# Performance work log

Measured on AMD Instinct MI355X. Metric: run time of the kernel, lower is better.

## Reference

```python
import jax, jax.numpy as jnp
import numpy as np

D_MODEL = 1024
N_HEAD = 16
B, C, S = 4, 4, 1024


def setup_inputs() -> dict:
    key = jax.random.key(0)
    ks = jax.random.split(key, 5)
    d = D_MODEL
    x = jax.random.normal(ks[0], (B, C, S, d), dtype=jnp.float32)
    scale = 1.0 / np.sqrt(d).astype(np.float32)

    def lin(k):
        return jax.random.normal(k, (d, d), dtype=jnp.float32) * scale

    return {
        "x": x,
        "wq": lin(ks[1]), "bq": jnp.zeros((d,), jnp.float32),
        "wk": lin(ks[2]), "bk": jnp.zeros((d,), jnp.float32),
        "wv": lin(ks[3]), "bv": jnp.zeros((d,), jnp.float32),
        "wo": lin(ks[4]), "bo": jnp.zeros((d,), jnp.float32),
    }


def reference(x, wq, bq, wk, bk, wv, bv, wo, bo):
    b, c, s, d = x.shape
    dh = d // N_HEAD
    nh = N_HEAD * c  # channels folded into heads, as in torch .view

    def proj(w, bias):
        # nn.Linear: y = x @ w.T + b  (w stored as [out, in])
        y = jnp.einsum('bcsd,ed->bcse', x, w) + bias
        # view(B, -1, n_head*C, d_head).transpose(1, 2) -> (B, nh, S, dh)
        return jnp.swapaxes(y.reshape(b, -1, nh, dh), 1, 2)

    # NOTE: original multiplies query by sqrt(d_head) (kept faithfully)
    q = proj(wq, bq) * jnp.sqrt(jnp.asarray(dh, x.dtype))
    k = proj(wk, bk)
    v = proj(wv, bv)

    attn = jax.nn.softmax(jnp.einsum('bhqd,bhkd->bhqk', q, k), axis=-1)
    o = jnp.einsum('bhqk,bhkd->bhqd', attn, v)          # (B, nh, S, dh)
    o = jnp.swapaxes(o, 1, 2).reshape(b, -1, N_HEAD * dh)  # (B, S*C, d)
    o = jnp.einsum('bnd,ed->bne', o, wo) + bo
    return o.reshape(b, c, -1, d)  # (B, C, S, d)
```

## Files before the change

### kernel.cpp

```cpp
#include <hip/hip_runtime.h>
#include <stdint.h>

typedef unsigned short u16;
typedef _Float16 f16;
typedef __attribute__((ext_vector_type(8))) _Float16 f16x8;
typedef __attribute__((ext_vector_type(4))) float f32x4;

__device__ __forceinline__ float exp2fast(float x) {
  return __builtin_amdgcn_exp2f(x);
}

__device__ __forceinline__ f32x4 mfma16(f16x8 a, f16x8 b, f32x4 c) {
  return __builtin_amdgcn_mfma_f32_16x16x32_f16(a, b, c, 0, 0, 0);
}

__device__ __forceinline__ u16 f2h(float f) {
  return __builtin_bit_cast(u16, (f16)f);
}

__device__ __forceinline__ void gld16(const void* g, void* l) {
  __builtin_amdgcn_global_load_lds(
      (const __attribute__((address_space(1))) unsigned int*)g,
      (__attribute__((address_space(3))) unsigned int*)l,
      16, 0, 0);
}

__global__ __launch_bounds__(256) void cvt_f32_f16(const float* __restrict__ in,
                                                   u16* __restrict__ out, int n4) {
  int stride = gridDim.x * blockDim.x;
  for (int i = blockIdx.x * blockDim.x + threadIdx.x; i < n4; i += stride) {
    float4 v = reinterpret_cast<const float4*>(in)[i];
    ushort4 o;
    o.x = f2h(v.x); o.y = f2h(v.y); o.z = f2h(v.z); o.w = f2h(v.w);
    reinterpret_cast<ushort4*>(out)[i] = o;
  }
}

struct GemmCore {
  u16* As;
  u16* Bs;
  const u16 *aS0, *aS1, *bS0, *bS1;
  u16 *aD0, *aD1, *bD0, *bD1;
  int aoff[4], boff[4];
};

__device__ __forceinline__ void core_init(GemmCore& c, u16* AsBase, u16* BsBase,
                                          const u16* A, const u16* B,
                                          int m0, int n0, int tid) {
  const int lane = tid & 63;
  const int wid = tid >> 6;
  const int wr = wid >> 1, wc = wid & 1;
  const int qd = lane >> 4, lm = lane & 15;

  c.As = AsBase; c.Bs = BsBase;
  const int srow = wid * 32 + (lane >> 2);
  const int sgran = (lane & 3) ^ ((lane >> 3) & 3);
  c.aS0 = A + (size_t)(m0 + srow) * 1024 + sgran * 8;
  c.aS1 = c.aS0 + (size_t)16 * 1024;
  c.bS0 = B + (size_t)(n0 + srow) * 1024 + sgran * 8;
  c.bS1 = c.bS0 + (size_t)16 * 1024;
  c.aD0 = AsBase + wid * 1024;       c.aD1 = c.aD0 + 512;
  c.bD0 = BsBase + wid * 1024;       c.bD1 = c.bD0 + 512;

  const int rg = (qd ^ ((lm >> 1) & 3)) * 8;
#pragma unroll
  for (int i = 0; i < 4; ++i) c.aoff[i] = (wr * 64 + i * 16 + lm) * 32 + rg;
#pragma unroll
  for (int j = 0; j < 4; ++j) c.boff[j] = (wc * 64 + j * 16 + lm) * 32 + rg;
}

__device__ __forceinline__ void core_stage(GemmCore& c, int buf) {
  const int d = buf * 4096;
  gld16(c.aS0, c.aD0 + d);
  gld16(c.aS1, c.aD1 + d);
  gld16(c.bS0, c.bD0 + d);
  gld16(c.bS1, c.bD1 + d);
}

__device__ __forceinline__ void core_advance(GemmCore& c) {
  c.aS0 += 32; c.aS1 += 32; c.bS0 += 32; c.bS1 += 32;
}

__device__ __forceinline__ void core_mfma(GemmCore& c, int buf, f32x4 (&acc)[4][4]) {
  const u16* aB = c.As + buf * 4096;
  const u16* bB = c.Bs + buf * 4096;
  f16x8 af[4], bf[4];
#pragma unroll
  for (int i = 0; i < 4; ++i)
    af[i] = *reinterpret_cast<const f16x8*>(aB + c.aoff[i]);
#pragma unroll
  for (int j = 0; j < 4; ++j)
    bf[j] = *reinterpret_cast<const f16x8*>(bB + c.boff[j]);
#pragma unroll
  for (int i = 0; i < 4; ++i)
#pragma unroll
    for (int j = 0; j < 4; ++j)
      acc[i][j] = mfma16(af[i], bf[j], acc[i][j]);
}

__global__ __launch_bounds__(256) void proj_qkv(
    const u16* __restrict__ xb,
    const u16* __restrict__ wqh, const u16* __restrict__ wkh, const u16* __restrict__ wvh,
    const float* __restrict__ bq, const float* __restrict__ bk, const float* __restrict__ bv,
    u16* __restrict__ Qf, u16* __restrict__ Kf, u16* __restrict__ Vt) {
  const int mat = blockIdx.z;
  const u16* __restrict__ w = (mat == 0) ? wqh : (mat == 1) ? wkh : wvh;
  const float* __restrict__ bias = (mat == 0) ? bq : (mat == 1) ? bk : bv;
  const int m0 = blockIdx.x * 128;
  const int n0 = blockIdx.y * 128;

  __shared__ __align__(16) u16 As[2][128 * 32];
  __shared__ __align__(16) u16 Bs[2][128 * 32];

  const int tid = threadIdx.x;
  const int lane = tid & 63;
  const int wid = tid >> 6;
  const int wr = wid >> 1, wc = wid & 1;
  const int qd = lane >> 4, lm = lane & 15;

  GemmCore c;
  core_init(c, &As[0][0], &Bs[0][0], xb, w, m0, n0, tid);

  f32x4 acc[4][4];
#pragma unroll
  for (int i = 0; i < 4; ++i)
#pragma unroll
    for (int j = 0; j < 4; ++j) acc[i][j] = (f32x4){0.f, 0.f, 0.f, 0.f};

  core_stage(c, 0);
  __syncthreads();

  int buf = 0;
  for (int kt = 0; kt < 31; ++kt) {
    core_advance(c);
    core_stage(c, buf ^ 1);
    core_mfma(c, buf, acc);
    __syncthreads();
    buf ^= 1;
  }
  core_mfma(c, buf, acc);

  const float scale = (mat == 0) ? 11.5415603f : 1.0f;
#pragma unroll
  for (int i = 0; i < 4; ++i) {
#pragma unroll
    for (int r = 0; r < 4; ++r) {
      int R = m0 + wr * 64 + i * 16 + qd * 4 + r;
      int bb = R >> 12, n = R & 4095;
      int cc = n >> 10, s = n & 1023;
      int rb = s & 3, t = s >> 2;
      int m = cc * 256 + t;
#pragma unroll
      for (int j = 0; j < 4; ++j) {
        int e = n0 + wc * 64 + j * 16 + lm;
        int head = e >> 6, jj = e & 63;
        int h = rb * 16 + head;
        float val = (acc[i][j][r] + bias[e]) * scale;
        u16 hv = f2h(val);
        if (mat == 2) {
          Vt[(((size_t)bb * 64 + h) * 64 + jj) * 1024 + m] = hv;
        } else {
          size_t idx = (((size_t)bb * 64 + h) * 1024 + m) * 64 + jj;
          if (mat == 0) Qf[idx] = hv;
          else          Kf[idx] = hv;
        }
      }
    }
  }
}

__device__ __forceinline__ f16x8 lds_frag(const u16* base, int row, int blk) {
  return *reinterpret_cast<const f16x8*>(base + row * 64 + ((blk ^ (row & 7)) << 3));
}

__device__ __forceinline__ void stage_kv(const u16* __restrict__ Kh,
                                         const u16* __restrict__ Vh, int kc,
                                         u16* KsB, u16* VsB, int wv, int lane) {
  const int l8 = lane >> 3, sl = lane & 7;
  const int rb = wv * 16;
#pragma unroll
  for (int it = 0; it < 2; ++it) {
    int row = rb + it * 8 + l8;
    int gsl = sl ^ l8;
    gld16(Kh + (size_t)(kc * 64 + row) * 64 + gsl * 8, KsB + (rb + it * 8) * 64);
    gld16(Vh + (size_t)row * 1024 + kc * 64 + gsl * 8, VsB + (rb + it * 8) * 64);
  }
}

__global__ __launch_bounds__(256) void attn_kernel(
    const u16* __restrict__ Qf, const u16* __restrict__ Kf,
    const u16* __restrict__ Vt, u16* __restrict__ Of) {
  const int wgid = (blockIdx.x & 7) * 256 + (blockIdx.x >> 3);
  const int bh = wgid >> 3;
  const int m0 = (wgid & 7) * 128;
  const int b = bh >> 6, h = bh & 63;
  const int tid = threadIdx.x, lane = tid & 63, wv = tid >> 6;
  const int qd = lane >> 4, lm = lane & 15;

  __shared__ __align__(16) u16 Ks[2][64 * 64];
  __shared__ __align__(16) u16 Vs[2][64 * 64];

  const size_t hb = (size_t)(b * 64 + h);
  const u16* __restrict__ Qh = Qf + hb * 65536;
  const u16* __restrict__ Kh = Kf + hb * 65536;
  const u16* __restrict__ Vh = Vt + hb * 65536;

  f16x8 qf[2][2];
#pragma unroll
  for (int im = 0; im < 2; ++im)
#pragma unroll
    for (int ks = 0; ks < 2; ++ks)
      qf[im][ks] = *reinterpret_cast<const f16x8*>(
          Qh + (size_t)(m0 + wv * 32 + im * 16 + lm) * 64 + ks * 32 + qd * 8);

  f32x4 oa[2][4];
  float mrow[2] = {-1e30f, -1e30f};
  float lrow[2] = {0.f, 0.f};
#pragma unroll
  for (int im = 0; im < 2; ++im)
#pragma unroll
    for (int jf = 0; jf < 4; ++jf) oa[im][jf] = (f32x4){0.f, 0.f, 0.f, 0.f};

  stage_kv(Kh, Vh, 0, &Ks[0][0], &Vs[0][0], wv, lane);

  for (int kc = 0; kc < 16; ++kc) {
    const int buf = kc & 1;
    __syncthreads();
    if (kc + 1 < 16) stage_kv(Kh, Vh, kc + 1, &Ks[buf ^ 1][0], &Vs[buf ^ 1][0], wv, lane);

    f32x4 sc[2][4];
#pragma unroll
    for (int im = 0; im < 2; ++im)
#pragma unroll
      for (int nf = 0; nf < 4; ++nf) sc[im][nf] = (f32x4){0.f, 0.f, 0.f, 0.f};
#pragma unroll
    for (int ks = 0; ks < 2; ++ks) {
      f16x8 kfr[4];
#pragma unroll
      for (int nf = 0; nf < 4; ++nf)
        kfr[nf] = lds_frag(&Ks[buf][0], nf * 16 + lm, ks * 4 + qd);
#pragma unroll
      for (int im = 0; im < 2; ++im)
#pragma unroll
        for (int nf = 0; nf < 4; ++nf)
          sc[im][nf] = mfma16(kfr[nf], qf[im][ks], sc[im][nf]);
    }

    unsigned int pk[2][8];
#pragma unroll
    for (int im = 0; im < 2; ++im) {
      float pm = sc[im][0][0];
#pragma unroll
      for (int nf = 0; nf < 4; ++nf)
#pragma unroll
        for (int r = 0; r < 4; ++r) pm = fmaxf(pm, sc[im][nf][r]);
      pm = fmaxf(pm, __shfl_xor(pm, 16));
      pm = fmaxf(pm, __shfl_xor(pm, 32));
      if (__all(pm <= mrow[im] + 8.0f)) {
        float mn = mrow[im];
        float s = 0.f;
#pragma unroll
        for (int nf = 0; nf < 4; ++nf) {
          float p0 = exp2fast(sc[im][nf][0] - mn);
          float p1 = exp2fast(sc[im][nf][1] - mn);
          float p2 = exp2fast(sc[im][nf][2] - mn);
          float p3 = exp2fast(sc[im][nf][3] - mn);
          s += (p0 + p1) + (p2 + p3);
          pk[im][2 * nf + 0] = __builtin_bit_cast(unsigned int, __builtin_amdgcn_cvt_pkrtz(p0, p1));
          pk[im][2 * nf + 1] = __builtin_bit_cast(unsigned int, __builtin_amdgcn_cvt_pkrtz(p2, p3));
        }
        s += __shfl_xor(s, 16);
        s += __shfl_xor(s, 32);
        lrow[im] += s;
      } else {
        float mn = fmaxf(mrow[im], pm);
        float corr = exp2fast(mrow[im] - mn);
        mrow[im] = mn;
        float s = 0.f;
#pragma unroll
        for (int nf = 0; nf < 4; ++nf) {
          float p0 = exp2fast(sc[im][nf][0] - mn);
          float p1 = exp2fast(sc[im][nf][1] - mn);
          float p2 = exp2fast(sc[im][nf][2] - mn);
          float p3 = exp2fast(sc[im][nf][3] - mn);
          s += (p0 + p1) + (p2 + p3);
          pk[im][2 * nf + 0] = __builtin_bit_cast(unsigned int, __builtin_amdgcn_cvt_pkrtz(p0, p1));
          pk[im][2 * nf + 1] = __builtin_bit_cast(unsigned int, __builtin_amdgcn_cvt_pkrtz(p2, p3));
        }
        s += __shfl_xor(s, 16);
        s += __shfl_xor(s, 32);
        lrow[im] = lrow[im] * corr + s;
#pragma unroll
        for (int r = 0; r < 4; ++r) {
          float cb = __shfl(corr, qd * 4 + r);
#pragma unroll
          for (int jf = 0; jf < 4; ++jf) oa[im][jf][r] *= cb;
        }
      }
    }

#pragma unroll
    for (int ks = 0; ks < 2; ++ks) {
      f16x8 vfr[4];
#pragma unroll
      for (int jf = 0; jf < 4; ++jf)
        vfr[jf] = lds_frag(&Vs[buf][0], jf * 16 + lm, ks * 4 + qd);
#pragma unroll
      for (int im = 0; im < 2; ++im) {
        union { unsigned int w[4]; f16x8 hv; } pa;
#pragma unroll
        for (int w = 0; w < 4; ++w) {
          int srcl = (((2 * qd + (w >> 1)) & 3) << 4) + lm;
          unsigned int a0 = __shfl(pk[im][2 * (2 * ks + 0) + (w & 1)], srcl);
          unsigned int a1 = __shfl(pk[im][2 * (2 * ks + 1) + (w & 1)], srcl);
          pa.w[w] = (qd & 2) ? a1 : a0;
        }
#pragma unroll
        for (int jf = 0; jf < 4; ++jf)
          oa[im][jf] = mfma16(pa.hv, vfr[jf], oa[im][jf]);
      }
    }
  }

  const int rb = h >> 4, head = h & 15;
#pragma unroll
  for (int im = 0; im < 2; ++im) {
#pragma unroll
    for (int r = 0; r < 4; ++r) {
      float lb = __shfl(lrow[im], qd * 4 + r);
      float inv = 1.0f / lb;
      int mq = m0 + wv * 32 + im * 16 + qd * 4 + r;
      int c = mq >> 8, t = mq & 255;
      int s = t * 4 + rb;
      int n = c * 1024 + s;
#pragma unroll
      for (int jf = 0; jf < 4; ++jf) {
        int j = jf * 16 + lm;
        int f = head * 64 + j;
        Of[((size_t)b * 4096 + n) * 1024 + f] = f2h(oa[im][jf][r] * inv);
      }
    }
  }
}

__global__ __launch_bounds__(256) void out_gemm(
    const u16* __restrict__ Of, const u16* __restrict__ woh,
    const float* __restrict__ bo, float* __restrict__ out) {
  const int m0 = blockIdx.x * 128;
  const int n0 = blockIdx.y * 128;

  __shared__ __align__(16) u16 As[2][128 * 32];
  __shared__ __align__(16) u16 Bs[2][128 * 32];

  const int tid = threadIdx.x;
  const int lane = tid & 63;
  const int wid = tid >> 6;
  const int wr = wid >> 1, wc = wid & 1;
  const int qd = lane >> 4, lm = lane & 15;

  GemmCore c;
  core_init(c, &As[0][0], &Bs[0][0], Of, woh, m0, n0, tid);

  f32x4 acc[4][4];
#pragma unroll
  for (int i = 0; i < 4; ++i)
#pragma unroll
    for (int j = 0; j < 4; ++j) acc[i][j] = (f32x4){0.f, 0.f, 0.f, 0.f};

  core_stage(c, 0);
  __syncthreads();

  int buf = 0;
  for (int kt = 0; kt < 31; ++kt) {
    core_advance(c);
    core_stage(c, buf ^ 1);
    core_mfma(c, buf, acc);
    __syncthreads();
    buf ^= 1;
  }
  core_mfma(c, buf, acc);

#pragma unroll
  for (int i = 0; i < 4; ++i) {
#pragma unroll
    for (int r = 0; r < 4; ++r) {
      int R = m0 + wr * 64 + i * 16 + qd * 4 + r;
#pragma unroll
      for (int j = 0; j < 4; ++j) {
        int e = n0 + wc * 64 + j * 16 + lm;
        out[(size_t)R * 1024 + e] = acc[i][j][r] + bo[e];
      }
    }
  }
}

extern "C" void kernel_launch(void* const* d_in, const int* in_sizes, int n_in,
                              void* d_out, int out_size, void* d_ws, size_t ws_size,
                              hipStream_t stream) {
  const float* x  = (const float*)d_in[0];
  const float* wq = (const float*)d_in[1];
  const float* bq = (const float*)d_in[2];
  const float* wk = (const float*)d_in[3];
  const float* bk = (const float*)d_in[4];
  const float* wv = (const float*)d_in[5];
  const float* bv = (const float*)d_in[6];
  const float* wo = (const float*)d_in[7];
  const float* bo = (const float*)d_in[8];
  float* out = (float*)d_out;

  char* ws = (char*)d_ws;
  u16* xb  = (u16*)(ws + 0);
  u16* wqh = (u16*)(ws + 33554432);
  u16* wkh = (u16*)(ws + 35651584);
  u16* wvh = (u16*)(ws + 37748736);
  u16* woh = (u16*)(ws + 39845888);
  u16* Qfb = (u16*)(ws + 41943040);
  u16* Kfb = (u16*)(ws + 75497472);
  u16* Vtb = (u16*)(ws + 109051904);
  u16* Ofb = (u16*)(ws + 142606336);

  cvt_f32_f16<<<4096, 256, 0, stream>>>(x,  xb,  16777216 / 4);
  cvt_f32_f16<<<1024, 256, 0, stream>>>(wq, wqh, 1048576 / 4);
  cvt_f32_f16<<<1024, 256, 0, stream>>>(wk, wkh, 1048576 / 4);
  cvt_f32_f16<<<1024, 256, 0, stream>>>(wv, wvh, 1048576 / 4);
  cvt_f32_f16<<<1024, 256, 0, stream>>>(wo, woh, 1048576 / 4);

  proj_qkv<<<dim3(128, 8, 3), 256, 0, stream>>>(xb, wqh, wkh, wvh, bq, bk, bv,
                                                Qfb, Kfb, Vtb);
  attn_kernel<<<2048, 256, 0, stream>>>(Qfb, Kfb, Vtb, Ofb);
  out_gemm<<<dim3(128, 8), 256, 0, stream>>>(Ofb, woh, bo, out);
}
```

Baseline: 433.7 us.

## Single-buffer GEMM LDS, merge weight conversions, add MFMA priority hints

Both GEMM kernels drop LDS double buffering for a single buffer with two barriers per k-step, halving shared memory so more blocks can be resident per CU, at the cost of no longer overlapping loads with MFMA inside a block. The four weight conversion launches become one launch that picks its matrix from blockIdx.y, cutting launch overhead. The attention kernel wraps its MFMA sections in s_setprio hints so waves issuing matrix work get scheduling priority over waves doing softmax.

```diff
diff --git a/kernel.cpp b/kernel.cpp
--- a/kernel.cpp
+++ b/kernel.cpp
@@ -36,9 +36,25 @@
   }
 }
 
+struct Ptr8 {
+  const float *s0, *s1, *s2, *s3;
+  u16 *d0, *d1, *d2, *d3;
+};
+__global__ __launch_bounds__(256) void cvt4_f32_f16(Ptr8 p, int n4) {
+  const float* in = (blockIdx.y == 0) ? p.s0 : (blockIdx.y == 1) ? p.s1
+                    : (blockIdx.y == 2) ? p.s2 : p.s3;
+  u16* out = (blockIdx.y == 0) ? p.d0 : (blockIdx.y == 1) ? p.d1
+             : (blockIdx.y == 2) ? p.d2 : p.d3;
+  int stride = gridDim.x * blockDim.x;
+  for (int i = blockIdx.x * blockDim.x + threadIdx.x; i < n4; i += stride) {
+    float4 v = reinterpret_cast<const float4*>(in)[i];
+    ushort4 o;
+    o.x = f2h(v.x); o.y = f2h(v.y); o.z = f2h(v.z); o.w = f2h(v.w);
+    reinterpret_cast<ushort4*>(out)[i] = o;
+  }
+}
+
 struct GemmCore {
-  u16* As;
-  u16* Bs;
   const u16 *aS0, *aS1, *bS0, *bS1;
   u16 *aD0, *aD1, *bD0, *bD1;
   int aoff[4], boff[4];
@@ -52,7 +68,6 @@
   const int wr = wid >> 1, wc = wid & 1;
   const int qd = lane >> 4, lm = lane & 15;
 
-  c.As = AsBase; c.Bs = BsBase;
   const int srow = wid * 32 + (lane >> 2);
   const int sgran = (lane & 3) ^ ((lane >> 3) & 3);
   c.aS0 = A + (size_t)(m0 + srow) * 1024 + sgran * 8;
@@ -69,28 +84,26 @@
   for (int j = 0; j < 4; ++j) c.boff[j] = (wc * 64 + j * 16 + lm) * 32 + rg;
 }
 
-__device__ __forceinline__ void core_stage(GemmCore& c, int buf) {
-  const int d = buf * 4096;
-  gld16(c.aS0, c.aD0 + d);
-  gld16(c.aS1, c.aD1 + d);
-  gld16(c.bS0, c.bD0 + d);
-  gld16(c.bS1, c.bD1 + d);
+__device__ __forceinline__ void core_stage(GemmCore& c) {
+  gld16(c.aS0, c.aD0);
+  gld16(c.aS1, c.aD1);
+  gld16(c.bS0, c.bD0);
+  gld16(c.bS1, c.bD1);
 }
 
 __device__ __forceinline__ void core_advance(GemmCore& c) {
   c.aS0 += 32; c.aS1 += 32; c.bS0 += 32; c.bS1 += 32;
 }
 
-__device__ __forceinline__ void core_mfma(GemmCore& c, int buf, f32x4 (&acc)[4][4]) {
-  const u16* aB = c.As + buf * 4096;
-  const u16* bB = c.Bs + buf * 4096;
+__device__ __forceinline__ void core_mfma(GemmCore& c, const u16* AsBase, const u16* BsBase,
+                                          f32x4 (&acc)[4][4]) {
   f16x8 af[4], bf[4];
 #pragma unroll
   for (int i = 0; i < 4; ++i)
-    af[i] = *reinterpret_cast<const f16x8*>(aB + c.aoff[i]);
+    af[i] = *reinterpret_cast<const f16x8*>(AsBase + c.aoff[i]);
 #pragma unroll
   for (int j = 0; j < 4; ++j)
-    bf[j] = *reinterpret_cast<const f16x8*>(bB + c.boff[j]);
+    bf[j] = *reinterpret_cast<const f16x8*>(BsBase + c.boff[j]);
 #pragma unroll
   for (int i = 0; i < 4; ++i)
 #pragma unroll
@@ -109,8 +122,8 @@
   const int m0 = blockIdx.x * 128;
   const int n0 = blockIdx.y * 128;
 
-  __shared__ __align__(16) u16 As[2][128 * 32];
-  __shared__ __align__(16) u16 Bs[2][128 * 32];
+  __shared__ __align__(16) u16 As[128 * 32];
+  __shared__ __align__(16) u16 Bs[128 * 32];
 
   const int tid = threadIdx.x;
   const int lane = tid & 63;
@@ -119,7 +132,7 @@
   const int qd = lane >> 4, lm = lane & 15;
 
   GemmCore c;
-  core_init(c, &As[0][0], &Bs[0][0], xb, w, m0, n0, tid);
+  core_init(c, As, Bs, xb, w, m0, n0, tid);
 
   f32x4 acc[4][4];
 #pragma unroll
@@ -127,18 +140,14 @@
 #pragma unroll
     for (int j = 0; j < 4; ++j) acc[i][j] = (f32x4){0.f, 0.f, 0.f, 0.f};
 
-  core_stage(c, 0);
-  __syncthreads();
-
-  int buf = 0;
-  for (int kt = 0; kt < 31; ++kt) {
-    core_advance(c);
-    core_stage(c, buf ^ 1);
-    core_mfma(c, buf, acc);
+  core_stage(c);
+
+  for (int kt = 0; kt < 32; ++kt) {
     __syncthreads();
-    buf ^= 1;
-  }
-  core_mfma(c, buf, acc);
+    core_mfma(c, As, Bs, acc);
+    __syncthreads();
+    if (kt + 1 < 32) { core_advance(c); core_stage(c); }
+  }
 
   const float scale = (mat == 0) ? 11.5415603f : 1.0f;
 #pragma unroll
@@ -233,6 +242,7 @@
     for (int im = 0; im < 2; ++im)
 #pragma unroll
       for (int nf = 0; nf < 4; ++nf) sc[im][nf] = (f32x4){0.f, 0.f, 0.f, 0.f};
+    __builtin_amdgcn_s_setprio(1);
 #pragma unroll
     for (int ks = 0; ks < 2; ++ks) {
       f16x8 kfr[4];
@@ -245,6 +255,7 @@
         for (int nf = 0; nf < 4; ++nf)
           sc[im][nf] = mfma16(kfr[nf], qf[im][ks], sc[im][nf]);
     }
+    __builtin_amdgcn_s_setprio(0);
 
     unsigned int pk[2][8];
 #pragma unroll
@@ -315,9 +326,11 @@
           unsigned int a1 = __shfl(pk[im][2 * (2 * ks + 1) + (w & 1)], srcl);
           pa.w[w] = (qd & 2) ? a1 : a0;
         }
+        __builtin_amdgcn_s_setprio(1);
 #pragma unroll
         for (int jf = 0; jf < 4; ++jf)
           oa[im][jf] = mfma16(pa.hv, vfr[jf], oa[im][jf]);
+        __builtin_amdgcn_s_setprio(0);
       }
     }
   }
@@ -349,8 +362,8 @@
   const int m0 = blockIdx.x * 128;
   const int n0 = blockIdx.y * 128;
 
-  __shared__ __align__(16) u16 As[2][128 * 32];
-  __shared__ __align__(16) u16 Bs[2][128 * 32];
+  __shared__ __align__(16) u16 As[128 * 32];
+  __shared__ __align__(16) u16 Bs[128 * 32];
 
   const int tid = threadIdx.x;
   const int lane = tid & 63;
@@ -359,7 +372,7 @@
   const int qd = lane >> 4, lm = lane & 15;
 
   GemmCore c;
-  core_init(c, &As[0][0], &Bs[0][0], Of, woh, m0, n0, tid);
+  core_init(c, As, Bs, Of, woh, m0, n0, tid);
 
   f32x4 acc[4][4];
 #pragma unroll
@@ -367,18 +380,14 @@
 #pragma unroll
     for (int j = 0; j < 4; ++j) acc[i][j] = (f32x4){0.f, 0.f, 0.f, 0.f};
 
-  core_stage(c, 0);
-  __syncthreads();
-
-  int buf = 0;
-  for (int kt = 0; kt < 31; ++kt) {
-    core_advance(c);
-    core_stage(c, buf ^ 1);
-    core_mfma(c, buf, acc);
+  core_stage(c);
+
+  for (int kt = 0; kt < 32; ++kt) {
     __syncthreads();
-    buf ^= 1;
-  }
-  core_mfma(c, buf, acc);
+    core_mfma(c, As, Bs, acc);
+    __syncthreads();
+    if (kt + 1 < 32) { core_advance(c); core_stage(c); }
+  }
 
 #pragma unroll
   for (int i = 0; i < 4; ++i) {
@@ -419,11 +428,9 @@
   u16* Vtb = (u16*)(ws + 109051904);
   u16* Ofb = (u16*)(ws + 142606336);
 
-  cvt_f32_f16<<<4096, 256, 0, stream>>>(x,  xb,  16777216 / 4);
-  cvt_f32_f16<<<1024, 256, 0, stream>>>(wq, wqh, 1048576 / 4);
-  cvt_f32_f16<<<1024, 256, 0, stream>>>(wk, wkh, 1048576 / 4);
-  cvt_f32_f16<<<1024, 256, 0, stream>>>(wv, wvh, 1048576 / 4);
-  cvt_f32_f16<<<1024, 256, 0, stream>>>(wo, woh, 1048576 / 4);
+  cvt_f32_f16<<<4096, 256, 0, stream>>>(x, xb, 16777216 / 4);
+  Ptr8 p { wq, wk, wv, wo, wqh, wkh, wvh, woh };
+  cvt4_f32_f16<<<dim3(256, 4), 256, 0, stream>>>(p, 1048576 / 4);
 
   proj_qkv<<<dim3(128, 8, 3), 256, 0, stream>>>(xb, wqh, wkh, wvh, bq, bk, bv,
                                                 Qfb, Kfb, Vtb);
```

Measured after the change: 415.7 us. 1.04x faster.
